# Performance work log

Measured on AMD Instinct MI355X. Metric: run time of the kernel, lower is better.

## Reference

```python
import jax, jax.numpy as jnp
import numpy as np

# Sizes (must match setup_inputs)
N = 1024      # total residues (2 structures x 512)
B = 2         # num_structid
RPS = 512     # residues per sample
P = 32        # n_protein_patches
E_AB = B * P * P
E_ab = 131072 # downsampled residue-residue edges
DIM = 256
PDIM = 128
NB = 15       # distance RBF basis count
EPS = 1e-6


def _fourier(x, f):
    # GaussianFourierEncoding1D: x [..., 1], f [m] -> [..., 2m]
    ang = 2.0 * jnp.pi * x * f
    return jnp.concatenate([jnp.sin(ang), jnp.cos(ang)], axis=-1)


def _gelu_mlp(x, w1, b1, w2, b2):
    return jnp.dot(jax.nn.gelu(jnp.dot(x, w1) + b1), w2) + b2


def _frames(coords):
    # get_frame_matrix from N, CA, C atoms via Gram-Schmidt; coords [N,3,3]
    a, b, c = coords[:, 0], coords[:, 1], coords[:, 2]
    v1 = c - b
    v2 = a - b
    e1 = v1 / (jnp.linalg.norm(v1, axis=-1, keepdims=True) + EPS)
    u2 = v2 - e1 * jnp.sum(e1 * v2, axis=-1, keepdims=True)
    e2 = u2 / (jnp.linalg.norm(u2, axis=-1, keepdims=True) + EPS)
    e3 = jnp.cross(e1, e2)
    R = jnp.stack([e1, e2, e3], axis=-1)  # columns are the frame axes
    return R, b


def setup_inputs() -> dict:
    key = jax.random.key(0)
    ks = jax.random.split(key, 16)

    def lin(k, i, o):
        return (jax.random.normal(k, (i, o), jnp.float32) / np.sqrt(i)).astype(jnp.float32)

    # per-sample index offsets so gathers stay within each structure
    off_ab = (jnp.arange(E_ab) // (E_ab // B)).astype(jnp.int32) * RPS
    gather_idx_ab_a = jax.random.randint(ks[0], (E_ab,), 0, RPS, jnp.int32) + off_ab
    gather_idx_ab_b = jax.random.randint(ks[1], (E_ab,), 0, RPS, jnp.int32) + off_ab
    off_pid = (jnp.arange(B * P) // P).astype(jnp.int32) * RPS
    gather_idx_pid_a = jax.random.randint(ks[2], (B * P,), 0, RPS, jnp.int32) + off_pid

    return {
        "res_embedding_in": jax.random.normal(ks[3], (N, DIM), jnp.float32),
        "timestep_encoding_prot": jax.random.uniform(ks[4], (N, 1), jnp.float32),
        "input_protein_coords": jax.random.normal(ks[5], (N, 3, 3), jnp.float32) * 3.0,
        "time_freq": jax.random.normal(ks[6], (16,), jnp.float32),
        "chain_freq": jax.random.normal(ks[7], (PDIM // 4,), jnp.float32),
        "w1_res": lin(ks[8], DIM + 32, DIM),
        "b1_res": jnp.zeros((DIM,), jnp.float32),
        "w2_res": lin(ks[9], DIM, DIM),
        "b2_res": jnp.zeros((DIM,), jnp.float32),
        "w_geom": lin(ks[10], NB + 9 + 3, PDIM),
        "w1_edge": lin(ks[11], PDIM + PDIM // 2 + 2 * DIM, DIM),
        "b1_edge": jnp.zeros((DIM,), jnp.float32),
        "w2_edge": lin(ks[12], DIM, PDIM),
        "b2_edge": jnp.zeros((PDIM,), jnp.float32),
        "residue_index": (jnp.arange(N, dtype=jnp.int32) % 256),
        "res_chain_id": (jnp.arange(N, dtype=jnp.int32) // 256),
        "gather_idx_ab_a": gather_idx_ab_a,
        "gather_idx_ab_b": gather_idx_ab_b,
        "gather_idx_pid_a": gather_idx_pid_a,
    }


def reference(res_embedding_in, timestep_encoding_prot, input_protein_coords,
              time_freq, chain_freq,
              w1_res, b1_res, w2_res, b2_res,
              w_geom,
              w1_edge, b1_edge, w2_edge, b2_edge,
              residue_index, res_chain_id,
              gather_idx_ab_a, gather_idx_ab_b, gather_idx_pid_a):
    # residue representation: res_in_mlp(cat(emb, time_enc)) + emb
    te = _fourier(timestep_encoding_prot, time_freq)  # [N, 32]
    rep = _gelu_mlp(jnp.concatenate([res_embedding_in, te], axis=-1),
                    w1_res, b1_res, w2_res, b2_res) + res_embedding_in

    # patch-grid (AB) edge expansion, then merged edge list (ab first, AB second)
    pid = gather_idx_pid_a.reshape(B, P)
    AB_a = jnp.broadcast_to(pid[:, :, None], (B, P, P)).reshape(-1)
    AB_b = jnp.broadcast_to(pid[:, None, :], (B, P, P)).reshape(-1)
    src = jnp.concatenate([gather_idx_ab_a, AB_a])
    dst = jnp.concatenate([gather_idx_ab_b, AB_b])

    # chain relative positional encoding (_compute_chain_pe)
    ri = residue_index.astype(jnp.float32)
    disp = (ri[src] - ri[dst]) / 8.0                        # [E]
    rope = _fourier(disp[:, None], chain_freq) / (jnp.abs(disp) + 1.0)[:, None]
    rope = rope * (res_chain_id[src] == res_chain_id[dst])[:, None]  # [E, PDIM//2]

    # relative geometry encoding from backbone frames
    R, t = _frames(input_protein_coords)
    d = t[dst] - t[src]                                     # [E, 3]
    dist = jnp.sqrt(jnp.sum(d * d, axis=-1) + EPS)
    local = jnp.einsum('eik,ei->ek', R[src], d) / (dist + 1.0)[:, None]
    relrot = jnp.einsum('eia,eib->eab', R[src], R[dst]).reshape(-1, 9)
    centers = jnp.linspace(0.0, 20.0, NB)
    sig = 20.0 / NB
    rbf = jnp.exp(-0.5 * ((dist[:, None] - centers) / sig) ** 2)
    geom = jnp.dot(jnp.concatenate([rbf, relrot, local], axis=-1), w_geom)  # [E, PDIM]

    # pp_edge_embed(cat(geom, chain_pe, rep[src], rep[dst]))
    edge_in = jnp.concatenate([geom, rope, rep[src], rep[dst]], axis=-1)
    edge_reps = _gelu_mlp(edge_in, w1_edge, b1_edge, w2_edge, b2_edge)  # [E, PDIM]
    return edge_reps
```

## Files before the change

kernel.cpp:

```cpp
#include <hip/hip_runtime.h>


typedef __attribute__((ext_vector_type(8))) short short8;
typedef __attribute__((ext_vector_type(4))) float f32x4;

#define TWO_PI 6.283185307179586f
#define E_AB_TOT 131072

#define WS_RT    0
#define WS_REPB  49152
#define WS_W1F   573440
#define WS_W2F   884736
#define WS_PS    950272
#define WS_PD    1998848

__device__ __forceinline__ unsigned short f2bf(float x){
  unsigned int u = __float_as_uint(x);
  u += 0x7fffu + ((u >> 16) & 1u);
  return (unsigned short)(u >> 16);
}

__device__ __forceinline__ unsigned int pack_bf16(float lo, float hi){
  unsigned int ul = __float_as_uint(lo), uh = __float_as_uint(hi);
  ul += 0x7fffu + ((ul >> 16) & 1u);
  uh += 0x7fffu + ((uh >> 16) & 1u);
  return __builtin_amdgcn_perm(uh, ul, 0x07060302);
}

__device__ __forceinline__ float gelu_s(float x){
  float s = x * x;
  float w = x * __builtin_fmaf(-0.1029437f, s, -2.30220847f);
  float e = __builtin_exp2f(w);
  return x * __builtin_amdgcn_rcpf(1.0f + e);
}

__global__ __launch_bounds__(256) void prep_k(
    const float* __restrict__ emb, const float* __restrict__ ts,
    const float* __restrict__ tf,  const float* __restrict__ w1,
    const float* __restrict__ b1,  const float* __restrict__ w2,
    const float* __restrict__ b2,  unsigned short* __restrict__ repb,
    const float* __restrict__ coords, float* __restrict__ RT,
    const float* __restrict__ wg, const float* __restrict__ w1e,
    unsigned short* __restrict__ w1f,
    const float* __restrict__ w2e, unsigned short* __restrict__ w2f){
  __shared__ float xt[288 * 12];
  __shared__ float ht[256 * 12];
  int blk = blockIdx.x, tid = threadIdx.x;
  if (blk < 256){
    int n0 = blk * 4;
    #pragma unroll
    for (int nd = 0; nd < 4; ++nd)
      xt[tid * 12 + nd] = emb[(n0 + nd) * 256 + tid];
    if (tid < 128){
      int nd = tid >> 5, j = tid & 31;
      float ang = TWO_PI * ts[n0 + nd] * tf[j & 15];
      float s, c; __sincosf(ang, &s, &c);
      xt[(256 + j) * 12 + nd] = (j < 16) ? s : c;
    }
    __syncthreads();
    float acc[4];
    float bias1 = b1[tid];
    #pragma unroll
    for (int nd = 0; nd < 4; ++nd) acc[nd] = bias1;
    #pragma unroll 8
    for (int k = 0; k < 288; ++k){
      float w = w1[k * 256 + tid];
      f32x4 xa = *(const f32x4*)&xt[k * 12];
      acc[0] += xa[0]*w; acc[1] += xa[1]*w; acc[2] += xa[2]*w; acc[3] += xa[3]*w;
    }
    #pragma unroll
    for (int nd = 0; nd < 4; ++nd) ht[tid * 12 + nd] = gelu_s(acc[nd]);
    __syncthreads();
    float acc2[4];
    float bias2 = b2[tid];
    #pragma unroll
    for (int nd = 0; nd < 4; ++nd) acc2[nd] = bias2;
    #pragma unroll 8
    for (int k = 0; k < 256; ++k){
      float w = w2[k * 256 + tid];
      f32x4 ha = *(const f32x4*)&ht[k * 12];
      acc2[0] += ha[0]*w; acc2[1] += ha[1]*w; acc2[2] += ha[2]*w; acc2[3] += ha[3]*w;
    }
    #pragma unroll
    for (int nd = 0; nd < 4; ++nd)
      repb[(n0 + nd) * 256 + tid] = f2bf(acc2[nd] + xt[tid * 12 + nd]);
  } else if (blk < 260){
    int n = (blk - 256) * 256 + tid;
    const float* p = coords + n * 9;
    float ax=p[0],ay=p[1],az=p[2], bx=p[3],by=p[4],bz=p[5], cx=p[6],cy=p[7],cz=p[8];
    float v1x=cx-bx, v1y=cy-by, v1z=cz-bz;
    float v2x=ax-bx, v2y=ay-by, v2z=az-bz;
    float n1 = sqrtf(v1x*v1x+v1y*v1y+v1z*v1z) + 1e-6f;
    float e1x=v1x/n1, e1y=v1y/n1, e1z=v1z/n1;
    float dp = e1x*v2x + e1y*v2y + e1z*v2z;
    float u2x=v2x-e1x*dp, u2y=v2y-e1y*dp, u2z=v2z-e1z*dp;
    float n2 = sqrtf(u2x*u2x+u2y*u2y+u2z*u2z) + 1e-6f;
    float e2x=u2x/n2, e2y=u2y/n2, e2z=u2z/n2;
    float* r = RT + n * 12;
    r[0]=e1x; r[1]=e2x; r[2]=e1y*e2z - e1z*e2y;
    r[3]=e1y; r[4]=e2y; r[5]=e1z*e2x - e1x*e2z;
    r[6]=e1z; r[7]=e2z; r[8]=e1x*e2y - e1y*e2x;
    r[9]=bx;  r[10]=by; r[11]=bz;
  } else if (blk < 276){
    int u = (blk - 260) * 4 + (tid >> 6);
    int lane = tid & 63;
    int s = u >> 3, c = u & 7;
    int n  = c * 16 + (lane & 15);
    int kb = s * 32 + (lane >> 4) * 8;
    unsigned short* o = w2f + (((s * 8 + c) * 64) + lane) * 8;
    unsigned short vals[8];
    #pragma unroll
    for (int j = 0; j < 8; ++j)
      vals[j] = f2bf(w2e[(kb + j) * 128 + n]);
    *(uint4*)o = *(const uint4*)vals;
  } else if (blk < 348){
    int u = 16 + (blk - 276) * 4 + (tid >> 6);
    int lane = tid & 63;
    int s = u >> 4, c = u & 15;
    int n  = c * 16 + (lane & 15);
    int kb = s * 32 + (lane >> 4) * 8;
    unsigned short* o = w1f + (((s * 16 + c) * 64) + lane) * 8;
    unsigned short vals[8];
    for (int j = 0; j < 8; ++j){
      int k = kb + j;
      float val;
      if (k < 91)       val = w1e[(128 + k - 27)  * 256 + n];
      else if (k < 96)  val = 0.f;
      else if (k < 352) val = w1e[(192 + k - 96)  * 256 + n];
      else              val = w1e[(448 + k - 352) * 256 + n];
      vals[j] = f2bf(val);
    }
    *(uint4*)o = *(const uint4*)vals;
  } else {
    int c = blk - 348;
    int n0 = c * 16;
    float* slab = xt;
    float* res  = ht;
    #pragma unroll
    for (int i = 0; i < 8; ++i){
      int idx = tid + 256 * i;
      slab[idx] = w1e[(idx >> 4) * 256 + n0 + (idx & 15)];
    }
    __syncthreads();
    #pragma unroll
    for (int i = 0; i < 2; ++i){
      int o = tid + 256 * i;
      if (o < 432){
        int k = o >> 4, cc = o & 15;
        float acc = 0.f;
        for (int j2 = 0; j2 < 128; ++j2)
          acc += wg[k * 128 + j2] * slab[j2 * 16 + cc];
        res[o] = acc;
      }
    }
    __syncthreads();
    if (tid < 64){
      int lane = tid;
      int nn = lane & 15;
      int kb = (lane >> 4) * 8;
      unsigned short vals[8];
      #pragma unroll
      for (int j = 0; j < 8; ++j){
        int k = kb + j;
        float val = (k < 27) ? res[k * 16 + nn]
                             : w1e[(128 + k - 27) * 256 + n0 + nn];
        vals[j] = f2bf(val);
      }
      *(uint4*)(w1f + ((c * 64) + lane) * 8) = *(const uint4*)vals;
    }
  }
}

__global__ __launch_bounds__(512) void proj_k(
    const unsigned short* __restrict__ repb,
    const unsigned short* __restrict__ w1f,
    const float* __restrict__ b1e,
    float* __restrict__ ps, float* __restrict__ pd)
{
  int part = blockIdx.x & 1;
  int nt   = blockIdx.x >> 1;
  int tid  = threadIdx.x, w = tid >> 6, lane = tid & 63;
  int c0 = w * 2, lr = lane & 15, quad = lane >> 4;
  int n0g = nt * 64;
  const short8* w1f8 = (const short8*)w1f;
  f32x4 acc[8];
  #pragma unroll
  for (int i = 0; i < 8; ++i) acc[i] = (f32x4){0.f, 0.f, 0.f, 0.f};
  int sb = 3 + part * 8;
  #pragma unroll
  for (int s = 0; s < 8; ++s){
    short8 a0 = w1f8[((sb + s) * 16 + c0 + 0) * 64 + lane];
    short8 a1 = w1f8[((sb + s) * 16 + c0 + 1) * 64 + lane];
    #pragma unroll
    for (int t = 0; t < 4; ++t){
      short8 b = *(const short8*)(repb + (n0g + t * 16 + lr) * 256 + s * 32 + quad * 8);
      acc[t]     = __builtin_amdgcn_mfma_f32_16x16x32_bf16(a0, b, acc[t],     0, 0, 0);
      acc[4 + t] = __builtin_amdgcn_mfma_f32_16x16x32_bf16(a1, b, acc[4 + t], 0, 0, 0);
    }
  }
  float* out = part ? pd : ps;
  #pragma unroll
  for (int c = 0; c < 2; ++c){
    f32x4 add = (f32x4){0.f, 0.f, 0.f, 0.f};
    if (!part) add = *(const f32x4*)(b1e + (c0 + c) * 16 + quad * 4);
    #pragma unroll
    for (int t = 0; t < 4; ++t){
      f32x4 v = acc[c * 4 + t];
      v[0] += add[0]; v[1] += add[1]; v[2] += add[2]; v[3] += add[3];
      *(f32x4*)(out + (n0g + t * 16 + lr) * 256 + w * 32 + quad * 8 + c * 4) = v;
    }
  }
}

__global__ __launch_bounds__(512, 4) void edge_k(
    const float* __restrict__ RT,  const float* __restrict__ cf,
    const int* __restrict__ resi, const int* __restrict__ chain,
    const int* __restrict__ gia,  const int* __restrict__ gib,
    const int* __restrict__ pid,
    const unsigned short* __restrict__ w1f, const unsigned short* __restrict__ w2f,
    const float* __restrict__ ps, const float* __restrict__ pd,
    const float* __restrict__ bias2,
    float* __restrict__ outp)
{
  __shared__ __align__(16) char smem[36864];
  __shared__ __align__(16) float rtbuf[128][12];
  __shared__ float scD[64];
  __shared__ float scI[64];
  __shared__ int lsrc[64];
  __shared__ int ldst[64];

  int tid = threadIdx.x;
  int e0  = blockIdx.x * 64;

  if (tid < 64){
    int e = e0 + tid, s_, d_;
    if (e < E_AB_TOT){ s_ = gia[e]; d_ = gib[e]; }
    else {
      int i = e - E_AB_TOT;
      int b = i >> 10, w_ = i & 1023;
      s_ = pid[b * 32 + (w_ >> 5)];
      d_ = pid[b * 32 + (w_ & 31)];
    }
    lsrc[tid] = s_; ldst[tid] = d_;
    float disp = ((float)resi[s_] - (float)resi[d_]) * 0.125f;
    scD[tid] = disp;
    scI[tid] = (chain[s_] == chain[d_]) ? 1.f / (fabsf(disp) + 1.f) : 0.f;
  } else if (tid < 192){
    int r  = tid - 64;
    int e  = e0 + (r & 63);
    int node;
    if (e < E_AB_TOT){ node = (r < 64) ? gia[e] : gib[e]; }
    else {
      int i = e - E_AB_TOT;
      int b = i >> 10, w_ = i & 1023;
      node = (r < 64) ? pid[b * 32 + (w_ >> 5)] : pid[b * 32 + (w_ & 31)];
    }
    const f32x4* p = (const f32x4*)(RT + node * 12);
    f32x4* q = (f32x4*)(&rtbuf[r][0]);
    q[0] = p[0]; q[1] = p[1]; q[2] = p[2];
  }
  __syncthreads();

  int w    = tid >> 6, lane = tid & 63;
  int c0   = w * 2;
  int lr   = lane & 15;
  int quad = lane >> 4, qoff = quad * 16;

  {
    #pragma unroll
    for (int it = 0; it < 4; ++it){
      int v = it * 512 + tid, ed = v >> 5, j = v & 31;
      float ang = TWO_PI * scD[ed] * cf[j];
      float s, c; __sincosf(ang, &s, &c);
      float inv = scI[ed];
      unsigned short* row = (unsigned short*)(smem + ed * 208);
      row[27 + j] = f2bf(s * inv);
      row[59 + j] = f2bf(c * inv);
    }
    #pragma unroll
    for (int it = 0; it < 2; ++it){
      int v = it * 512 + tid, ed = v >> 4, c = v & 15;
      float tx = rtbuf[64 + ed][9]  - rtbuf[ed][9];
      float ty = rtbuf[64 + ed][10] - rtbuf[ed][10];
      float tz = rtbuf[64 + ed][11] - rtbuf[ed][11];
      float dist = sqrtf(tx*tx + ty*ty + tz*tz + 1e-6f);
      if (c < 15){
        float z = (dist - (float)c * (20.f / 14.f)) * (15.f / 20.f);
        ((unsigned short*)(smem + ed * 208))[c] = f2bf(__expf(-0.5f * z * z));
      }
    }
    #pragma unroll
    for (int it = 0; it < 2; ++it){
      int v = it * 512 + tid, ed = v >> 4, cc = v & 15;
      if (cc < 12){
        const float* Rs = &rtbuf[ed][0];
        const float* Rd = &rtbuf[64 + ed][0];
        float val;
        if (cc < 9){
          int a  = (cc >= 6) ? 2 : ((cc >= 3) ? 1 : 0);
          int b_ = cc - 3 * a;
          val = Rs[a]*Rd[b_] + Rs[3+a]*Rd[3+b_] + Rs[6+a]*Rd[6+b_];
        } else {
          int k = cc - 9;
          float tx = Rd[9]-Rs[9], ty = Rd[10]-Rs[10], tz = Rd[11]-Rs[11];
          float dist = sqrtf(tx*tx + ty*ty + tz*tz + 1e-6f);
          val = (Rs[k]*tx + Rs[3+k]*ty + Rs[6+k]*tz) / (dist + 1.f);
        }
        ((unsigned short*)(smem + ed * 208))[15 + cc] = f2bf(val);
      }
    }
    {
      int ed = tid >> 3, c8 = tid & 7;
      ((unsigned short*)(smem + ed * 208))[91 + c8] = 0;
    }
  }
  __syncthreads();

  f32x4 acc[8];
  #pragma unroll
  for (int i = 0; i < 8; ++i) acc[i] = (f32x4){0.f, 0.f, 0.f, 0.f};
  const short8* w1f8 = (const short8*)w1f;

  #pragma unroll
  for (int s = 0; s < 3; ++s){
    short8 a0 = w1f8[(s * 16 + c0 + 0) * 64 + lane];
    short8 a1 = w1f8[(s * 16 + c0 + 1) * 64 + lane];
    short8 be0 = *(const short8*)(smem + ( 0 + lr) * 208 + s * 64 + qoff);
    short8 be1 = *(const short8*)(smem + (16 + lr) * 208 + s * 64 + qoff);
    short8 be2 = *(const short8*)(smem + (32 + lr) * 208 + s * 64 + qoff);
    short8 be3 = *(const short8*)(smem + (48 + lr) * 208 + s * 64 + qoff);
    acc[0] = __builtin_amdgcn_mfma_f32_16x16x32_bf16(a0, be0, acc[0], 0, 0, 0);
    acc[1] = __builtin_amdgcn_mfma_f32_16x16x32_bf16(a0, be1, acc[1], 0, 0, 0);
    acc[2] = __builtin_amdgcn_mfma_f32_16x16x32_bf16(a0, be2, acc[2], 0, 0, 0);
    acc[3] = __builtin_amdgcn_mfma_f32_16x16x32_bf16(a0, be3, acc[3], 0, 0, 0);
    acc[4] = __builtin_amdgcn_mfma_f32_16x16x32_bf16(a1, be0, acc[4], 0, 0, 0);
    acc[5] = __builtin_amdgcn_mfma_f32_16x16x32_bf16(a1, be1, acc[5], 0, 0, 0);
    acc[6] = __builtin_amdgcn_mfma_f32_16x16x32_bf16(a1, be2, acc[6], 0, 0, 0);
    acc[7] = __builtin_amdgcn_mfma_f32_16x16x32_bf16(a1, be3, acc[7], 0, 0, 0);
  }

  int offS[4], offD[4];
  #pragma unroll
  for (int t = 0; t < 4; ++t){
    offS[t] = lsrc[t * 16 + lr] * 256 + w * 32 + quad * 8;
    offD[t] = ldst[t * 16 + lr] * 256 + w * 32 + quad * 8;
  }
  __syncthreads();

  {
    char* Hb = smem;
    #pragma unroll
    for (int c = 0; c < 2; ++c){
      f32x4 pv[4], qv[4];
      #pragma unroll
      for (int t = 0; t < 4; ++t){
        pv[t] = *(const f32x4*)(ps + offS[t] + c * 4);
        qv[t] = *(const f32x4*)(pd + offD[t] + c * 4);
      }
      int n = (c0 + c) * 16 + quad * 4;
      #pragma unroll
      for (int t = 0; t < 4; ++t){
        int e = t * 16 + lr;
        f32x4 s4 = acc[c * 4 + t];
        float v0 = gelu_s(s4[0] + pv[t][0] + qv[t][0]);
        float v1 = gelu_s(s4[1] + pv[t][1] + qv[t][1]);
        float v2 = gelu_s(s4[2] + pv[t][2] + qv[t][2]);
        float v3 = gelu_s(s4[3] + pv[t][3] + qv[t][3]);
        uint2 p; p.x = pack_bf16(v0, v1); p.y = pack_bf16(v2, v3);
        *(uint2*)(Hb + ((e * 512 + n * 2) ^ ((e & 7) << 4))) = p;
      }
    }
  }
  __syncthreads();

  int c2 = (w & 3) * 2;
  int eb = (w >> 2) * 32;
  int hx = (lr & 7) << 4;
  f32x4 acc2[4];
  #pragma unroll
  for (int i = 0; i < 4; ++i) acc2[i] = (f32x4){0.f, 0.f, 0.f, 0.f};
  const short8* w2f8 = (const short8*)w2f;
  #pragma unroll
  for (int s = 0; s < 8; ++s){
    short8 aa0 = w2f8[(s * 8 + c2 + 0) * 64 + lane];
    short8 aa1 = w2f8[(s * 8 + c2 + 1) * 64 + lane];
    short8 h0 = *(const short8*)(smem + (((eb +  0 + lr) * 512 + s * 64 + qoff) ^ hx));
    short8 h1 = *(const short8*)(smem + (((eb + 16 + lr) * 512 + s * 64 + qoff) ^ hx));
    acc2[0] = __builtin_amdgcn_mfma_f32_16x16x32_bf16(aa0, h0, acc2[0], 0, 0, 0);
    acc2[1] = __builtin_amdgcn_mfma_f32_16x16x32_bf16(aa0, h1, acc2[1], 0, 0, 0);
    acc2[2] = __builtin_amdgcn_mfma_f32_16x16x32_bf16(aa1, h0, acc2[2], 0, 0, 0);
    acc2[3] = __builtin_amdgcn_mfma_f32_16x16x32_bf16(aa1, h1, acc2[3], 0, 0, 0);
  }

  {
    int n0 = c2 * 16 + quad * 4;
    f32x4 bz0 = *(const f32x4*)(bias2 + n0);
    f32x4 bz1 = *(const f32x4*)(bias2 + n0 + 16);
    float* og = outp + (size_t)e0 * 128;
    #pragma unroll
    for (int t = 0; t < 2; ++t){
      int e = eb + t * 16 + lr;
      f32x4 v0, v1;
      v0[0] = acc2[t][0] + bz0[0]; v0[1] = acc2[t][1] + bz0[1];
      v0[2] = acc2[t][2] + bz0[2]; v0[3] = acc2[t][3] + bz0[3];
      v1[0] = acc2[2 + t][0] + bz1[0]; v1[1] = acc2[2 + t][1] + bz1[1];
      v1[2] = acc2[2 + t][2] + bz1[2]; v1[3] = acc2[2 + t][3] + bz1[3];
      *(f32x4*)(og + (size_t)e * 128 + n0)      = v0;
      *(f32x4*)(og + (size_t)e * 128 + n0 + 16) = v1;
    }
  }
}

extern "C" void kernel_launch(void* const* d_in, const int* in_sizes, int n_in,
                              void* d_out, int out_size, void* d_ws, size_t ws_size,
                              hipStream_t stream) {
  const float* emb    = (const float*)d_in[0];
  const float* ts     = (const float*)d_in[1];
  const float* coords = (const float*)d_in[2];
  const float* tf     = (const float*)d_in[3];
  const float* cf     = (const float*)d_in[4];
  const float* w1r    = (const float*)d_in[5];
  const float* b1r    = (const float*)d_in[6];
  const float* w2r    = (const float*)d_in[7];
  const float* b2r    = (const float*)d_in[8];
  const float* wg     = (const float*)d_in[9];
  const float* w1e    = (const float*)d_in[10];
  const float* b1e    = (const float*)d_in[11];
  const float* w2e    = (const float*)d_in[12];
  const float* b2e    = (const float*)d_in[13];
  const int* resi     = (const int*)d_in[14];
  const int* chain    = (const int*)d_in[15];
  const int* gia      = (const int*)d_in[16];
  const int* gib      = (const int*)d_in[17];
  const int* pid      = (const int*)d_in[18];

  char* ws = (char*)d_ws;
  float* RT            = (float*)(ws + WS_RT);
  unsigned short* REPB = (unsigned short*)(ws + WS_REPB);
  unsigned short* W1F  = (unsigned short*)(ws + WS_W1F);
  unsigned short* W2F  = (unsigned short*)(ws + WS_W2F);
  float* PS            = (float*)(ws + WS_PS);
  float* PD            = (float*)(ws + WS_PD);
  float* outp          = (float*)d_out;

  hipLaunchKernelGGL(prep_k, dim3(364), dim3(256), 0, stream,
                     emb, ts, tf, w1r, b1r, w2r, b2r, REPB,
                     coords, RT, wg, w1e, W1F, w2e, W2F);
  hipLaunchKernelGGL(proj_k, dim3(32), dim3(512), 0, stream,
                     REPB, W1F, b1e, PS, PD);
  hipLaunchKernelGGL(edge_k, dim3(2080), dim3(512), 0, stream,
                     RT, cf, resi, chain, gia, gib, pid, W1F, W2F, PS, PD,
                     b2e, outp);
}
```

Before: 202.8 us.

## Move residue MLP to a bf16 MFMA kernel and pad edge hidden tile

The residue embedding MLP, previously computed with scalar fp32 FMAs inside prep_k across 256 blocks, moves to a new mlp_k kernel. That kernel uses bf16 MFMA on pre-swizzled weight fragments produced by prep_k. The edge kernel's LDS hidden buffer drops the XOR swizzle in favour of a padded row stride of 560 bytes, and the ps/pd addressing is recomputed inline. This adds a fourth kernel launch and rounds the residue MLP inputs and hidden state to bf16.

```diff
diff --git a/kernel.cpp b/kernel.cpp
--- a/kernel.cpp
+++ b/kernel.cpp
@@ -13,6 +13,8 @@
 #define WS_W2F   884736
 #define WS_PS    950272
 #define WS_PD    1998848
+#define WS_W1RF  3047424
+#define WS_W2RF  3194880
 
 __device__ __forceinline__ unsigned short f2bf(float x){
   unsigned int u = __float_as_uint(x);
@@ -35,57 +37,17 @@
 }
 
 __global__ __launch_bounds__(256) void prep_k(
-    const float* __restrict__ emb, const float* __restrict__ ts,
-    const float* __restrict__ tf,  const float* __restrict__ w1,
-    const float* __restrict__ b1,  const float* __restrict__ w2,
-    const float* __restrict__ b2,  unsigned short* __restrict__ repb,
     const float* __restrict__ coords, float* __restrict__ RT,
     const float* __restrict__ wg, const float* __restrict__ w1e,
     unsigned short* __restrict__ w1f,
-    const float* __restrict__ w2e, unsigned short* __restrict__ w2f){
+    const float* __restrict__ w2e, unsigned short* __restrict__ w2f,
+    const float* __restrict__ w1r, unsigned short* __restrict__ w1rf,
+    const float* __restrict__ w2r, unsigned short* __restrict__ w2rf){
   __shared__ float xt[288 * 12];
   __shared__ float ht[256 * 12];
   int blk = blockIdx.x, tid = threadIdx.x;
-  if (blk < 256){
-    int n0 = blk * 4;
-    #pragma unroll
-    for (int nd = 0; nd < 4; ++nd)
-      xt[tid * 12 + nd] = emb[(n0 + nd) * 256 + tid];
-    if (tid < 128){
-      int nd = tid >> 5, j = tid & 31;
-      float ang = TWO_PI * ts[n0 + nd] * tf[j & 15];
-      float s, c; __sincosf(ang, &s, &c);
-      xt[(256 + j) * 12 + nd] = (j < 16) ? s : c;
-    }
-    __syncthreads();
-    float acc[4];
-    float bias1 = b1[tid];
-    #pragma unroll
-    for (int nd = 0; nd < 4; ++nd) acc[nd] = bias1;
-    #pragma unroll 8
-    for (int k = 0; k < 288; ++k){
-      float w = w1[k * 256 + tid];
-      f32x4 xa = *(const f32x4*)&xt[k * 12];
-      acc[0] += xa[0]*w; acc[1] += xa[1]*w; acc[2] += xa[2]*w; acc[3] += xa[3]*w;
-    }
-    #pragma unroll
-    for (int nd = 0; nd < 4; ++nd) ht[tid * 12 + nd] = gelu_s(acc[nd]);
-    __syncthreads();
-    float acc2[4];
-    float bias2 = b2[tid];
-    #pragma unroll
-    for (int nd = 0; nd < 4; ++nd) acc2[nd] = bias2;
-    #pragma unroll 8
-    for (int k = 0; k < 256; ++k){
-      float w = w2[k * 256 + tid];
-      f32x4 ha = *(const f32x4*)&ht[k * 12];
-      acc2[0] += ha[0]*w; acc2[1] += ha[1]*w; acc2[2] += ha[2]*w; acc2[3] += ha[3]*w;
-    }
-    #pragma unroll
-    for (int nd = 0; nd < 4; ++nd)
-      repb[(n0 + nd) * 256 + tid] = f2bf(acc2[nd] + xt[tid * 12 + nd]);
-  } else if (blk < 260){
-    int n = (blk - 256) * 256 + tid;
+  if (blk < 4){
+    int n = blk * 256 + tid;
     const float* p = coords + n * 9;
     float ax=p[0],ay=p[1],az=p[2], bx=p[3],by=p[4],bz=p[5], cx=p[6],cy=p[7],cz=p[8];
     float v1x=cx-bx, v1y=cy-by, v1z=cz-bz;
@@ -101,8 +63,8 @@
     r[3]=e1y; r[4]=e2y; r[5]=e1z*e2x - e1x*e2z;
     r[6]=e1z; r[7]=e2z; r[8]=e1x*e2y - e1y*e2x;
     r[9]=bx;  r[10]=by; r[11]=bz;
-  } else if (blk < 276){
-    int u = (blk - 260) * 4 + (tid >> 6);
+  } else if (blk < 20){
+    int u = (blk - 4) * 4 + (tid >> 6);
     int lane = tid & 63;
     int s = u >> 3, c = u & 7;
     int n  = c * 16 + (lane & 15);
@@ -113,8 +75,8 @@
     for (int j = 0; j < 8; ++j)
       vals[j] = f2bf(w2e[(kb + j) * 128 + n]);
     *(uint4*)o = *(const uint4*)vals;
-  } else if (blk < 348){
-    int u = 16 + (blk - 276) * 4 + (tid >> 6);
+  } else if (blk < 92){
+    int u = 16 + (blk - 20) * 4 + (tid >> 6);
     int lane = tid & 63;
     int s = u >> 4, c = u & 15;
     int n  = c * 16 + (lane & 15);
@@ -131,8 +93,8 @@
       vals[j] = f2bf(val);
     }
     *(uint4*)o = *(const uint4*)vals;
-  } else {
-    int c = blk - 348;
+  } else if (blk < 108){
+    int c = blk - 92;
     int n0 = c * 16;
     float* slab = xt;
     float* res  = ht;
@@ -168,6 +130,130 @@
       }
       *(uint4*)(w1f + ((c * 64) + lane) * 8) = *(const uint4*)vals;
     }
+  } else if (blk < 144){
+    int u = (blk - 108) * 4 + (tid >> 6);
+    int lane = tid & 63;
+    int s = u >> 4, c = u & 15;
+    int n  = c * 16 + (lane & 15);
+    int kb = s * 32 + (lane >> 4) * 8;
+    unsigned short* o = w1rf + (((s * 16 + c) * 64) + lane) * 8;
+    unsigned short vals[8];
+    #pragma unroll
+    for (int j = 0; j < 8; ++j)
+      vals[j] = f2bf(w1r[(kb + j) * 256 + n]);
+    *(uint4*)o = *(const uint4*)vals;
+  } else {
+    int u = (blk - 144) * 4 + (tid >> 6);
+    int lane = tid & 63;
+    int s = u >> 4, c = u & 15;
+    int n  = c * 16 + (lane & 15);
+    int kb = s * 32 + (lane >> 4) * 8;
+    unsigned short* o = w2rf + (((s * 16 + c) * 64) + lane) * 8;
+    unsigned short vals[8];
+    #pragma unroll
+    for (int j = 0; j < 8; ++j)
+      vals[j] = f2bf(w2r[(kb + j) * 256 + n]);
+    *(uint4*)o = *(const uint4*)vals;
+  }
+}
+
+__global__ __launch_bounds__(512) void mlp_k(
+    const float* __restrict__ emb, const float* __restrict__ ts,
+    const float* __restrict__ tf,
+    const unsigned short* __restrict__ w1rf, const float* __restrict__ b1r,
+    const unsigned short* __restrict__ w2rf, const float* __restrict__ b2r,
+    unsigned short* __restrict__ repb)
+{
+  __shared__ __align__(16) char X[32 * 592];
+  __shared__ __align__(16) char H1[32 * 512];
+  int tid = threadIdx.x;
+  int n0g = blockIdx.x * 32;
+
+  #pragma unroll
+  for (int i = 0; i < 4; ++i){
+    int idx = tid + 512 * i;
+    int row = idx >> 6, g = idx & 63;
+    f32x4 e = *(const f32x4*)(emb + (n0g + row) * 256 + g * 4);
+    uint2 p; p.x = pack_bf16(e[0], e[1]); p.y = pack_bf16(e[2], e[3]);
+    *(uint2*)(X + row * 592 + g * 8) = p;
+  }
+  {
+    int nd = tid >> 4, j = tid & 15;
+    float ang = TWO_PI * ts[n0g + nd] * tf[j];
+    float s, c; __sincosf(ang, &s, &c);
+    *(unsigned short*)(X + nd * 592 + 512 + 2 * j) = f2bf(s);
+    *(unsigned short*)(X + nd * 592 + 544 + 2 * j) = f2bf(c);
+  }
+  __syncthreads();
+
+  int w = tid >> 6, lane = tid & 63;
+  int c0 = w * 2, lr = lane & 15, quad = lane >> 4, qoff = quad * 16;
+
+  f32x4 acc[4];
+  #pragma unroll
+  for (int i = 0; i < 4; ++i) acc[i] = (f32x4){0.f, 0.f, 0.f, 0.f};
+  const short8* w1rf8 = (const short8*)w1rf;
+  #pragma unroll
+  for (int s = 0; s < 9; ++s){
+    short8 a0 = w1rf8[(s * 16 + c0 + 0) * 64 + lane];
+    short8 a1 = w1rf8[(s * 16 + c0 + 1) * 64 + lane];
+    short8 b0 = *(const short8*)(X + ( 0 + lr) * 592 + s * 64 + qoff);
+    short8 b1 = *(const short8*)(X + (16 + lr) * 592 + s * 64 + qoff);
+    acc[0] = __builtin_amdgcn_mfma_f32_16x16x32_bf16(a0, b0, acc[0], 0, 0, 0);
+    acc[1] = __builtin_amdgcn_mfma_f32_16x16x32_bf16(a0, b1, acc[1], 0, 0, 0);
+    acc[2] = __builtin_amdgcn_mfma_f32_16x16x32_bf16(a1, b0, acc[2], 0, 0, 0);
+    acc[3] = __builtin_amdgcn_mfma_f32_16x16x32_bf16(a1, b1, acc[3], 0, 0, 0);
+  }
+
+  #pragma unroll
+  for (int c = 0; c < 2; ++c){
+    int n = (c0 + c) * 16 + quad * 4;
+    f32x4 bz = *(const f32x4*)(b1r + n);
+    #pragma unroll
+    for (int t = 0; t < 2; ++t){
+      int node = t * 16 + lr;
+      f32x4 s4 = acc[c * 2 + t];
+      float v0 = gelu_s(s4[0] + bz[0]);
+      float v1 = gelu_s(s4[1] + bz[1]);
+      float v2 = gelu_s(s4[2] + bz[2]);
+      float v3 = gelu_s(s4[3] + bz[3]);
+      uint2 p; p.x = pack_bf16(v0, v1); p.y = pack_bf16(v2, v3);
+      *(uint2*)(H1 + ((node * 512 + n * 2) ^ ((node & 7) << 4))) = p;
+    }
+  }
+  __syncthreads();
+
+  f32x4 acc2[4];
+  #pragma unroll
+  for (int i = 0; i < 4; ++i) acc2[i] = (f32x4){0.f, 0.f, 0.f, 0.f};
+  const short8* w2rf8 = (const short8*)w2rf;
+  int hx = (lr & 7) << 4;
+  #pragma unroll
+  for (int s = 0; s < 8; ++s){
+    short8 a0 = w2rf8[(s * 16 + c0 + 0) * 64 + lane];
+    short8 a1 = w2rf8[(s * 16 + c0 + 1) * 64 + lane];
+    short8 b0 = *(const short8*)(H1 + ((( 0 + lr) * 512 + s * 64 + qoff) ^ hx));
+    short8 b1 = *(const short8*)(H1 + (((16 + lr) * 512 + s * 64 + qoff) ^ hx));
+    acc2[0] = __builtin_amdgcn_mfma_f32_16x16x32_bf16(a0, b0, acc2[0], 0, 0, 0);
+    acc2[1] = __builtin_amdgcn_mfma_f32_16x16x32_bf16(a0, b1, acc2[1], 0, 0, 0);
+    acc2[2] = __builtin_amdgcn_mfma_f32_16x16x32_bf16(a1, b0, acc2[2], 0, 0, 0);
+    acc2[3] = __builtin_amdgcn_mfma_f32_16x16x32_bf16(a1, b1, acc2[3], 0, 0, 0);
+  }
+
+  #pragma unroll
+  for (int c = 0; c < 2; ++c){
+    int n = (c0 + c) * 16 + quad * 4;
+    f32x4 bz = *(const f32x4*)(b2r + n);
+    #pragma unroll
+    for (int t = 0; t < 2; ++t){
+      int node = t * 16 + lr;
+      f32x4 e = *(const f32x4*)(emb + (n0g + node) * 256 + n);
+      f32x4 s4 = acc2[c * 2 + t];
+      uint2 p;
+      p.x = pack_bf16(s4[0] + bz[0] + e[0], s4[1] + bz[1] + e[1]);
+      p.y = pack_bf16(s4[2] + bz[2] + e[2], s4[3] + bz[3] + e[3]);
+      *(uint2*)(repb + (n0g + node) * 256 + n) = p;
+    }
   }
 }
 
@@ -201,13 +287,14 @@
   float* out = part ? pd : ps;
   #pragma unroll
   for (int c = 0; c < 2; ++c){
+    int n = (c0 + c) * 16 + quad * 4;
     f32x4 add = (f32x4){0.f, 0.f, 0.f, 0.f};
-    if (!part) add = *(const f32x4*)(b1e + (c0 + c) * 16 + quad * 4);
+    if (!part) add = *(const f32x4*)(b1e + n);
     #pragma unroll
     for (int t = 0; t < 4; ++t){
       f32x4 v = acc[c * 4 + t];
       v[0] += add[0]; v[1] += add[1]; v[2] += add[2]; v[3] += add[3];
-      *(f32x4*)(out + (n0g + t * 16 + lr) * 256 + w * 32 + quad * 8 + c * 4) = v;
+      *(f32x4*)(out + (n0g + t * 16 + lr) * 256 + n) = v;
     }
   }
 }
@@ -222,7 +309,7 @@
     const float* __restrict__ bias2,
     float* __restrict__ outp)
 {
-  __shared__ __align__(16) char smem[36864];
+  __shared__ __align__(16) char smem[35840];
   __shared__ __align__(16) float rtbuf[128][12];
   __shared__ float scD[64];
   __shared__ float scI[64];
@@ -260,11 +347,6 @@
     q[0] = p[0]; q[1] = p[1]; q[2] = p[2];
   }
   __syncthreads();
-
-  int w    = tid >> 6, lane = tid & 63;
-  int c0   = w * 2;
-  int lr   = lane & 15;
-  int quad = lane >> 4, qoff = quad * 16;
 
   {
     #pragma unroll
@@ -316,6 +398,10 @@
   }
   __syncthreads();
 
+  int w    = tid >> 6, lane = tid & 63;
+  int c0   = w * 2;
+  int lr   = lane & 15;
+  int quad = lane >> 4, qoff = quad * 16;
   f32x4 acc[8];
   #pragma unroll
   for (int i = 0; i < 8; ++i) acc[i] = (f32x4){0.f, 0.f, 0.f, 0.f};
@@ -338,26 +424,19 @@
     acc[6] = __builtin_amdgcn_mfma_f32_16x16x32_bf16(a1, be2, acc[6], 0, 0, 0);
     acc[7] = __builtin_amdgcn_mfma_f32_16x16x32_bf16(a1, be3, acc[7], 0, 0, 0);
   }
-
-  int offS[4], offD[4];
-  #pragma unroll
-  for (int t = 0; t < 4; ++t){
-    offS[t] = lsrc[t * 16 + lr] * 256 + w * 32 + quad * 8;
-    offD[t] = ldst[t * 16 + lr] * 256 + w * 32 + quad * 8;
-  }
   __syncthreads();
 
   {
     char* Hb = smem;
     #pragma unroll
     for (int c = 0; c < 2; ++c){
+      int n = (c0 + c) * 16 + quad * 4;
       f32x4 pv[4], qv[4];
       #pragma unroll
       for (int t = 0; t < 4; ++t){
-        pv[t] = *(const f32x4*)(ps + offS[t] + c * 4);
-        qv[t] = *(const f32x4*)(pd + offD[t] + c * 4);
+        pv[t] = *(const f32x4*)(ps + (size_t)lsrc[t * 16 + lr] * 256 + n);
+        qv[t] = *(const f32x4*)(pd + (size_t)ldst[t * 16 + lr] * 256 + n);
       }
-      int n = (c0 + c) * 16 + quad * 4;
       #pragma unroll
       for (int t = 0; t < 4; ++t){
         int e = t * 16 + lr;
@@ -367,7 +446,7 @@
         float v2 = gelu_s(s4[2] + pv[t][2] + qv[t][2]);
         float v3 = gelu_s(s4[3] + pv[t][3] + qv[t][3]);
         uint2 p; p.x = pack_bf16(v0, v1); p.y = pack_bf16(v2, v3);
-        *(uint2*)(Hb + ((e * 512 + n * 2) ^ ((e & 7) << 4))) = p;
+        *(uint2*)(Hb + e * 560 + n * 2) = p;
       }
     }
   }
@@ -375,7 +454,6 @@
 
   int c2 = (w & 3) * 2;
   int eb = (w >> 2) * 32;
-  int hx = (lr & 7) << 4;
   f32x4 acc2[4];
   #pragma unroll
   for (int i = 0; i < 4; ++i) acc2[i] = (f32x4){0.f, 0.f, 0.f, 0.f};
@@ -384,8 +462,8 @@
   for (int s = 0; s < 8; ++s){
     short8 aa0 = w2f8[(s * 8 + c2 + 0) * 64 + lane];
     short8 aa1 = w2f8[(s * 8 + c2 + 1) * 64 + lane];
-    short8 h0 = *(const short8*)(smem + (((eb +  0 + lr) * 512 + s * 64 + qoff) ^ hx));
-    short8 h1 = *(const short8*)(smem + (((eb + 16 + lr) * 512 + s * 64 + qoff) ^ hx));
+    short8 h0 = *(const short8*)(smem + (eb +  0 + lr) * 560 + s * 64 + qoff);
+    short8 h1 = *(const short8*)(smem + (eb + 16 + lr) * 560 + s * 64 + qoff);
     acc2[0] = __builtin_amdgcn_mfma_f32_16x16x32_bf16(aa0, h0, acc2[0], 0, 0, 0);
     acc2[1] = __builtin_amdgcn_mfma_f32_16x16x32_bf16(aa0, h1, acc2[1], 0, 0, 0);
     acc2[2] = __builtin_amdgcn_mfma_f32_16x16x32_bf16(aa1, h0, acc2[2], 0, 0, 0);
@@ -441,11 +519,14 @@
   unsigned short* W2F  = (unsigned short*)(ws + WS_W2F);
   float* PS            = (float*)(ws + WS_PS);
   float* PD            = (float*)(ws + WS_PD);
+  unsigned short* W1RF = (unsigned short*)(ws + WS_W1RF);
+  unsigned short* W2RF = (unsigned short*)(ws + WS_W2RF);
   float* outp          = (float*)d_out;
 
-  hipLaunchKernelGGL(prep_k, dim3(364), dim3(256), 0, stream,
-                     emb, ts, tf, w1r, b1r, w2r, b2r, REPB,
-                     coords, RT, wg, w1e, W1F, w2e, W2F);
+  hipLaunchKernelGGL(prep_k, dim3(176), dim3(256), 0, stream,
+                     coords, RT, wg, w1e, W1F, w2e, W2F, w1r, W1RF, w2r, W2RF);
+  hipLaunchKernelGGL(mlp_k, dim3(32), dim3(512), 0, stream,
+                     emb, ts, tf, W1RF, b1r, W2RF, b2r, REPB);
   hipLaunchKernelGGL(proj_k, dim3(32), dim3(512), 0, stream,
                      REPB, W1F, b1e, PS, PD);
   hipLaunchKernelGGL(edge_k, dim3(2080), dim3(512), 0, stream,
```

Result: faster. 192.6 us (-5.0%).
